# Optimization experiments

Hardware: AMD Instinct MI355X
Metric: run time of the kernel (lower is better)

Reference implementation:

```python
import jax, jax.numpy as jnp
import numpy as np

DIM = 1024
NUM_HEADS = 16


def setup_inputs() -> dict:
    key = jax.random.key(0)
    ks = jax.random.split(key, 6)
    B, N, C = 2, 2048, DIM
    x = jax.random.normal(ks[0], (B, N, C), dtype=jnp.float32)
    # torch nn.Linear weights have shape (out, in); qkv_bias=False, proj has bias
    wq = jax.random.normal(ks[1], (C, C), dtype=jnp.float32) * 0.02
    wk = jax.random.normal(ks[2], (C, C), dtype=jnp.float32) * 0.02
    wv = jax.random.normal(ks[3], (C, C), dtype=jnp.float32) * 0.02
    wp = jax.random.normal(ks[4], (C, C), dtype=jnp.float32) * 0.02
    bp = jax.random.normal(ks[5], (C,), dtype=jnp.float32) * 0.02
    return {"x": x, "wq": wq, "wk": wk, "wv": wv, "wp": wp, "bp": bp}


def reference(x, wq, wk, wv, wp, bp):
    B, N, C = x.shape
    H = NUM_HEADS
    D = C // H
    scale = D ** (-0.5)
    # projections (torch Linear: x @ W.T), split heads -> (B, H, N, D)
    q = (x @ wq.T).reshape(B, N, H, D).transpose(0, 2, 1, 3)
    k = (x @ wk.T).reshape(B, N, H, D).transpose(0, 2, 1, 3)
    v = (x @ wv.T).reshape(B, N, H, D).transpose(0, 2, 1, 3)
    # average keys over sequence -> (B, H, D)
    k_avg = k.mean(axis=2)
    # per-position logits against the single averaged key -> (B, H, N)
    z = jnp.einsum('bhnd,bhd->bhn', q, k_avg) * scale
    attn = jax.nn.softmax(z, axis=-1)  # (B, H, N); dropout is identity at eval
    # build circulant matrix: roll_weights[..., i, j] = attn[..., (j - i) mod N]
    pos = jnp.arange(N)
    idx = (pos[None, :] - pos[:, None]) % N  # (N, N)
    roll_weights = attn[:, :, idx]  # (B, H, N, N) gather-built circulant
    out = jnp.einsum('bhij,bhjd->bhid', roll_weights, v)  # (B, H, N, D)
    out = out.transpose(0, 2, 1, 3).reshape(B, N, C)
    return out @ wp.T + bp
```

## Files before the change

kernel.cpp:

```cpp
#include <hip/hip_runtime.h>
#include <stdint.h>

typedef unsigned short u16;
typedef __bf16 bf16x8 __attribute__((ext_vector_type(8)));
typedef float f32x4 __attribute__((ext_vector_type(4)));

static constexpr int kDim   = 1024;
static constexpr int kHeads = 16;
static constexpr int kN     = 2048;
static constexpr int kB     = 2;
static constexpr int kTok   = 4096;

static constexpr size_t OFF_XB   = 0;
static constexpr size_t OFF_VT   = OFF_XB   + (size_t)kTok*kDim*2;
static constexpr size_t OFF_OC   = OFF_VT   + (size_t)kTok*kDim*2;
static constexpr size_t OFF_WVB  = OFF_OC   + (size_t)kTok*kDim*2;
static constexpr size_t OFF_WPB  = OFF_WVB  + (size_t)kDim*kDim*2;
static constexpr size_t OFF_PART = OFF_WPB  + (size_t)kDim*kDim*2;
static constexpr size_t OFF_WZ   = OFF_PART + (size_t)kB*16*kDim*4;
static constexpr size_t OFF_Z    = OFF_WZ   + (size_t)kB*kHeads*kDim*4;
static constexpr size_t OFF_ATTN = OFF_Z    + (size_t)kB*kHeads*kN*4;
static constexpr int kAttnStride = 2064;

__device__ __forceinline__ u16 f2bf(float f) {
  unsigned int u = __builtin_bit_cast(unsigned int, f);
  u = (u + 0x7FFFu + ((u >> 16) & 1u)) >> 16;
  return (u16)u;
}

__device__ __forceinline__ void gload_lds16(const void* g, void* l) {
  __builtin_amdgcn_global_load_lds(
      (const __attribute__((address_space(1))) unsigned int*)g,
      (__attribute__((address_space(3))) unsigned int*)l, 16, 0, 0);
}

__global__ void cvtx_xsum_kernel(const float* __restrict__ x, u16* __restrict__ xb,
                                 float* __restrict__ part) {
  int bid = blockIdx.x;
  int cc = bid & 3, nc = (bid >> 2) & 15, b = bid >> 6;
  int tid = threadIdx.x, rg = tid >> 6, cl = tid & 63;
  int col = cc * 256 + cl * 4;
  size_t base = (size_t)b * kN + nc * 128;
  float4 s = make_float4(0.f, 0.f, 0.f, 0.f);
  for (int n = rg; n < 128; n += 4) {
    size_t idx = (base + n) * kDim + col;
    float4 v = *reinterpret_cast<const float4*>(&x[idx]);
    unsigned int lo = (unsigned int)f2bf(v.x) | ((unsigned int)f2bf(v.y) << 16);
    unsigned int hi = (unsigned int)f2bf(v.z) | ((unsigned int)f2bf(v.w) << 16);
    *reinterpret_cast<uint2*>(&xb[idx]) = make_uint2(lo, hi);
    s.x += v.x; s.y += v.y; s.z += v.z; s.w += v.w;
  }
  __shared__ float ps[4][256];
  ps[rg][cl * 4 + 0] = s.x; ps[rg][cl * 4 + 1] = s.y;
  ps[rg][cl * 4 + 2] = s.z; ps[rg][cl * 4 + 3] = s.w;
  __syncthreads();
  float tot = ps[0][tid] + ps[1][tid] + ps[2][tid] + ps[3][tid];
  part[((size_t)(b * 16 + nc)) * kDim + cc * 256 + tid] = tot;
}

__global__ void cvtw_kernel(const float* __restrict__ wv, const float* __restrict__ wp,
                            u16* __restrict__ out) {
  int i = blockIdx.x * 256 + threadIdx.x;
  const int half = kDim * kDim / 4;
  float4 f = (i < half) ? reinterpret_cast<const float4*>(wv)[i]
                        : reinterpret_cast<const float4*>(wp)[i - half];
  unsigned int lo = (unsigned int)f2bf(f.x) | ((unsigned int)f2bf(f.y) << 16);
  unsigned int hi = (unsigned int)f2bf(f.z) | ((unsigned int)f2bf(f.w) << 16);
  reinterpret_cast<uint2*>(out)[i] = make_uint2(lo, hi);
}

__global__ void kavgwz_kernel(const float* __restrict__ part, const float* __restrict__ wk,
                              const float* __restrict__ wq, float* __restrict__ wz) {
  int bh = blockIdx.x;
  int b = bh >> 4, h = bh & 15, tid = threadIdx.x;
  __shared__ float xsl[1024];
  __shared__ float kl[64];
  {
    f32x4 s = (f32x4){0.f, 0.f, 0.f, 0.f};
    for (int ch = 0; ch < 16; ++ch)
      s += *reinterpret_cast<const f32x4*>(&part[((size_t)(b * 16 + ch)) * kDim + tid * 4]);
    *reinterpret_cast<f32x4*>(&xsl[tid * 4]) = s;
  }
  __syncthreads();
  int d = tid >> 2, pt = tid & 3;
  const float* wkr = wk + (size_t)(h * 64 + d) * kDim;
  float s = 0.f;
  for (int k = pt; k < kDim; k += 4) s += xsl[k] * wkr[k];
  s += __shfl_xor(s, 1);
  s += __shfl_xor(s, 2);
  if (pt == 0) kl[d] = s * (1.0f / (float)kN);
  __syncthreads();
  float a0 = 0.f, a1 = 0.f, a2 = 0.f, a3 = 0.f;
  const float* wqb = wq + (size_t)h * 64 * kDim + tid;
  for (int dd = 0; dd < 64; ++dd) {
    float kd = kl[dd];
    const float* r = wqb + (size_t)dd * kDim;
    a0 += kd * r[0]; a1 += kd * r[256]; a2 += kd * r[512]; a3 += kd * r[768];
  }
  const float scale = 0.125f;
  float* o = wz + (size_t)bh * kDim + tid;
  o[0] = a0 * scale; o[256] = a1 * scale; o[512] = a2 * scale; o[768] = a3 * scale;
}

__global__ void z_kernel(const float* __restrict__ x, const float* __restrict__ wz,
                         float* __restrict__ z) {
  int blk = blockIdx.x;
  int b = blk >> 11, n = blk & 2047;
  __shared__ float xr[kDim];
  int tid = threadIdx.x, wid = tid >> 6, lane = tid & 63;
  reinterpret_cast<float4*>(xr)[tid] = reinterpret_cast<const float4*>(x + (size_t)blk * kDim)[tid];
  __syncthreads();
#pragma unroll
  for (int hh = 0; hh < 4; ++hh) {
    int h = wid * 4 + hh;
    const float* wzr = wz + (size_t)(b * kHeads + h) * kDim;
    float s = 0.f;
    for (int k = lane; k < kDim; k += 64) s += xr[k] * wzr[k];
#pragma unroll
    for (int off = 32; off; off >>= 1) s += __shfl_xor(s, off);
    if (lane == 0) z[(size_t)(b * kHeads + h) * kN + n] = s;
  }
}

__global__ void softmax_kernel(const float* __restrict__ z, u16* __restrict__ attn2) {
  int row = blockIdx.x, tid = threadIdx.x;
  int lane = tid & 63, wid = tid >> 6;
  const float* zr = z + (size_t)row * kN;
  float v[8];
  float mx = -1e30f;
#pragma unroll
  for (int j = 0; j < 8; ++j) { v[j] = zr[tid + j * 256]; mx = fmaxf(mx, v[j]); }
#pragma unroll
  for (int off = 32; off; off >>= 1) mx = fmaxf(mx, __shfl_xor(mx, off));
  __shared__ float redm[4], reds[4];
  if (lane == 0) redm[wid] = mx;
  __syncthreads();
  mx = fmaxf(fmaxf(redm[0], redm[1]), fmaxf(redm[2], redm[3]));
  float s = 0.f;
#pragma unroll
  for (int j = 0; j < 8; ++j) { v[j] = __expf(v[j] - mx); s += v[j]; }
#pragma unroll
  for (int off = 32; off; off >>= 1) s += __shfl_xor(s, off);
  if (lane == 0) reds[wid] = s;
  __syncthreads();
  s = reds[0] + reds[1] + reds[2] + reds[3];
  float inv = 1.0f / s;
  u16* out = attn2 + (size_t)row * kAttnStride;
#pragma unroll
  for (int j = 0; j < 8; ++j) out[tid + j * 256] = f2bf(v[j] * inv);
  if (tid < 8) out[2048 + tid] = f2bf(v[0] * inv);
}

template <int MODE>
__global__ __launch_bounds__(256, 2)
void gemm_bt_kernel(const u16* __restrict__ A, const u16* __restrict__ B,
                    void* __restrict__ Cout, const float* __restrict__ bias, int K) {
  __shared__ __align__(16) u16 As[2][128 * 64];
  __shared__ __align__(16) u16 Bs[2][64 * 64];
  int tid = threadIdx.x, lane = tid & 63, wid = tid >> 6;
  int wm = wid >> 1, wn = wid & 1;
  int lrow = lane & 15, kg = lane >> 4;
  int m0 = blockIdx.y * 128, n0 = blockIdx.x * 64;

  auto stage = [&](int buf, int k0) {
#pragma unroll
    for (int it = 0; it < 4; ++it) {
      int bchunk = it * 256 + wid * 64;
      int chunk = bchunk + lane;
      int row = chunk >> 3, cb = chunk & 7;
      int cs = cb ^ (row & 7);
      gload_lds16(A + (size_t)(m0 + row) * K + k0 + cs * 8, &As[buf][bchunk * 8]);
    }
#pragma unroll
    for (int it = 0; it < 2; ++it) {
      int bchunk = it * 256 + wid * 64;
      int chunk = bchunk + lane;
      int row = chunk >> 3, cb = chunk & 7;
      int cs = cb ^ (row & 7);
      gload_lds16(B + (size_t)(n0 + row) * K + k0 + cs * 8, &Bs[buf][bchunk * 8]);
    }
  };

  f32x4 acc[4][2];
#pragma unroll
  for (int i = 0; i < 4; ++i)
#pragma unroll
    for (int j = 0; j < 2; ++j) acc[i][j] = (f32x4){0.f, 0.f, 0.f, 0.f};

  stage(0, 0);
  __syncthreads();
  int buf = 0;
  for (int k0 = 0; k0 < K; k0 += 64) {
    if (k0 + 64 < K) stage(buf ^ 1, k0 + 64);
#pragma unroll
    for (int ks = 0; ks < 2; ++ks) {
      bf16x8 af[4], bfv[2];
#pragma unroll
      for (int mf = 0; mf < 4; ++mf) {
        int r = wm * 64 + mf * 16 + lrow;
        int c = (ks * 4 + kg) ^ (r & 7);
        af[mf] = *reinterpret_cast<const bf16x8*>(&As[buf][r * 64 + c * 8]);
      }
#pragma unroll
      for (int nf = 0; nf < 2; ++nf) {
        int r = wn * 32 + nf * 16 + lrow;
        int c = (ks * 4 + kg) ^ (r & 7);
        bfv[nf] = *reinterpret_cast<const bf16x8*>(&Bs[buf][r * 64 + c * 8]);
      }
#pragma unroll
      for (int mf = 0; mf < 4; ++mf)
#pragma unroll
        for (int nf = 0; nf < 2; ++nf)
          acc[mf][nf] = __builtin_amdgcn_mfma_f32_16x16x32_bf16(af[mf], bfv[nf], acc[mf][nf], 0, 0, 0);
    }
    __syncthreads();
    buf ^= 1;
  }

  if (MODE == 0) {
    u16* vT = (u16*)Cout;
#pragma unroll
    for (int mf = 0; mf < 4; ++mf) {
      int row0 = m0 + wm * 64 + mf * 16 + kg * 4;
      int bb = row0 >> 11, u = row0 & 2047;
#pragma unroll
      for (int nf = 0; nf < 2; ++nf) {
        int col = n0 + wn * 32 + nf * 16 + lrow;
        f32x4 a = acc[mf][nf];
        unsigned int lo = (unsigned int)f2bf(a.x) | ((unsigned int)f2bf(a.y) << 16);
        unsigned int hi = (unsigned int)f2bf(a.z) | ((unsigned int)f2bf(a.w) << 16);
        *reinterpret_cast<uint2*>(&vT[((size_t)(bb * kDim + col)) * kN + u]) = make_uint2(lo, hi);
      }
    }
  } else {
    float* y = (float*)Cout;
#pragma unroll
    for (int nf = 0; nf < 2; ++nf) {
      int col = n0 + wn * 32 + nf * 16 + lrow;
      float bv = bias[col];
#pragma unroll
      for (int mf = 0; mf < 4; ++mf) {
        int row0 = m0 + wm * 64 + mf * 16 + kg * 4;
        f32x4 a = acc[mf][nf];
        y[(size_t)(row0 + 0) * kDim + col] = a.x + bv;
        y[(size_t)(row0 + 1) * kDim + col] = a.y + bv;
        y[(size_t)(row0 + 2) * kDim + col] = a.z + bv;
        y[(size_t)(row0 + 3) * kDim + col] = a.w + bv;
      }
    }
  }
}

__global__ __launch_bounds__(256, 2)
void conv_kernel(const u16* __restrict__ vT, const u16* __restrict__ attn2,
                 u16* __restrict__ oc) {
  static constexpr int RS = 2056;
  __shared__ __align__(16) u16 reps[8 * RS];
  __shared__ __align__(16) u16 vts[2][64 * 64];
  int tid = threadIdx.x, lane = tid & 63, wid = tid >> 6;
  int wm = wid >> 1, wn = wid & 1;
  int lrow = lane & 15, kg = lane >> 4;
  int i0 = blockIdx.x * 128;
  int bh = blockIdx.y;
  int b = bh >> 4, h = bh & 15;

  const u16* arow = attn2 + (size_t)bh * kAttnStride;
  for (int p = 0; p < 8; ++p)
    for (int j = tid; j < 2048; j += 256) reps[p * RS + j] = arow[j + p];

  auto stage = [&](int buf, int u0) {
#pragma unroll
    for (int it = 0; it < 2; ++it) {
      int bchunk = it * 256 + wid * 64;
      int chunk = bchunk + lane;
      int d = chunk >> 3, cb = chunk & 7;
      int cs = cb ^ (d & 7);
      gload_lds16(vT + (size_t)(bh * 64 + d) * kN + u0 + cs * 8, &vts[buf][bchunk * 8]);
    }
  };

  f32x4 acc[2][4];
#pragma unroll
  for (int i = 0; i < 2; ++i)
#pragma unroll
    for (int j = 0; j < 4; ++j) acc[i][j] = (f32x4){0.f, 0.f, 0.f, 0.f};

  stage(0, 0);
  __syncthreads();
  int buf = 0;
  for (int u0 = 0; u0 < kN; u0 += 64) {
    if (u0 + 64 < kN) stage(buf ^ 1, u0 + 64);
#pragma unroll
    for (int ks = 0; ks < 2; ++ks) {
      bf16x8 af[2], bfv[4];
#pragma unroll
      for (int mf = 0; mf < 2; ++mf) {
        int r = wm * 32 + mf * 16 + lrow;
        int c = (ks * 4 + kg) ^ (r & 7);
        af[mf] = *reinterpret_cast<const bf16x8*>(&vts[buf][r * 64 + c * 8]);
      }
#pragma unroll
      for (int nf = 0; nf < 4; ++nf) {
        int i = i0 + wn * 64 + nf * 16 + lrow;
        int s = (u0 + ks * 32 + kg * 8 - i) & 2047;
        int p = s & 7;
        bfv[nf] = *reinterpret_cast<const bf16x8*>(&reps[p * RS + (s & ~7)]);
      }
#pragma unroll
      for (int mf = 0; mf < 2; ++mf)
#pragma unroll
        for (int nf = 0; nf < 4; ++nf)
          acc[mf][nf] = __builtin_amdgcn_mfma_f32_16x16x32_bf16(af[mf], bfv[nf], acc[mf][nf], 0, 0, 0);
    }
    __syncthreads();
    buf ^= 1;
  }

#pragma unroll
  for (int mf = 0; mf < 2; ++mf) {
    int d = wm * 32 + mf * 16 + kg * 4;
#pragma unroll
    for (int nf = 0; nf < 4; ++nf) {
      int i = i0 + wn * 64 + nf * 16 + lrow;
      f32x4 a = acc[mf][nf];
      unsigned int lo = (unsigned int)f2bf(a.x) | ((unsigned int)f2bf(a.y) << 16);
      unsigned int hi = (unsigned int)f2bf(a.z) | ((unsigned int)f2bf(a.w) << 16);
      *reinterpret_cast<uint2*>(&oc[((size_t)(b * kN + i)) * kDim + h * 64 + d]) = make_uint2(lo, hi);
    }
  }
}

extern "C" void kernel_launch(void* const* d_in, const int* in_sizes, int n_in,
                              void* d_out, int out_size, void* d_ws, size_t ws_size,
                              hipStream_t stream) {
  const float* x  = (const float*)d_in[0];
  const float* wq = (const float*)d_in[1];
  const float* wk = (const float*)d_in[2];
  const float* wv = (const float*)d_in[3];
  const float* wp = (const float*)d_in[4];
  const float* bp = (const float*)d_in[5];
  char* ws = (char*)d_ws;

  u16*   xb    = (u16*)(ws + OFF_XB);
  u16*   vTb   = (u16*)(ws + OFF_VT);
  u16*   ocb   = (u16*)(ws + OFF_OC);
  u16*   wvb   = (u16*)(ws + OFF_WVB);
  float* part  = (float*)(ws + OFF_PART);
  float* wz    = (float*)(ws + OFF_WZ);
  float* z     = (float*)(ws + OFF_Z);
  u16*   attn2 = (u16*)(ws + OFF_ATTN);
  u16*   wpb   = (u16*)(ws + OFF_WPB);

  cvtx_xsum_kernel<<<128, 256, 0, stream>>>(x, xb, part);
  cvtw_kernel<<<2048, 256, 0, stream>>>(wv, wp, wvb);
  kavgwz_kernel<<<32, 256, 0, stream>>>(part, wk, wq, wz);
  z_kernel<<<4096, 256, 0, stream>>>(x, wz, z);
  softmax_kernel<<<32, 256, 0, stream>>>(z, attn2);

  gemm_bt_kernel<0><<<dim3(16, 32), 256, 0, stream>>>(xb, wvb, vTb, nullptr, kDim);
  conv_kernel<<<dim3(16, 32), 256, 0, stream>>>(vTb, attn2, ocb);
  gemm_bt_kernel<1><<<dim3(16, 32), 256, 0, stream>>>(ocb, wpb, (float*)d_out, bp, kDim);
}
```

Before: 230.1 us.

## Split averaged-key and wz computation into three wider-parallel kernels

Replaces the single 32-block kavgwz kernel with three launches: a reduction of partial column sums, a 2048-block kernel computing each averaged-key element with one wavefront, and a 256-block kernel projecting the averaged key through wq. The old kernel ran only 32 blocks, each streaming a 64x1024 slice of wk and wq, which leaves most compute units idle. The split spreads that weight traffic across many more blocks, at the cost of two extra kernel launches and small intermediate buffers in the workspace.

```diff
diff --git a/kernel.cpp b/kernel.cpp
--- a/kernel.cpp
+++ b/kernel.cpp
@@ -17,7 +17,9 @@
 static constexpr size_t OFF_WVB  = OFF_OC   + (size_t)kTok*kDim*2;
 static constexpr size_t OFF_WPB  = OFF_WVB  + (size_t)kDim*kDim*2;
 static constexpr size_t OFF_PART = OFF_WPB  + (size_t)kDim*kDim*2;
-static constexpr size_t OFF_WZ   = OFF_PART + (size_t)kB*16*kDim*4;
+static constexpr size_t OFF_XS   = OFF_PART + (size_t)kB*16*kDim*4;
+static constexpr size_t OFF_KAVG = OFF_XS   + (size_t)kB*kDim*4;
+static constexpr size_t OFF_WZ   = OFF_KAVG + (size_t)kB*kHeads*64*4;
 static constexpr size_t OFF_Z    = OFF_WZ   + (size_t)kB*kHeads*kDim*4;
 static constexpr size_t OFF_ATTN = OFF_Z    + (size_t)kB*kHeads*kN*4;
 static constexpr int kAttnStride = 2064;
@@ -69,37 +71,41 @@
   reinterpret_cast<uint2*>(out)[i] = make_uint2(lo, hi);
 }
 
-__global__ void kavgwz_kernel(const float* __restrict__ part, const float* __restrict__ wk,
-                              const float* __restrict__ wq, float* __restrict__ wz) {
-  int bh = blockIdx.x;
-  int b = bh >> 4, h = bh & 15, tid = threadIdx.x;
-  __shared__ float xsl[1024];
+__global__ void xsumred_kernel(const float* __restrict__ part, float* __restrict__ xsum) {
+  int i = blockIdx.x * 256 + threadIdx.x;
+  int b = i >> 10, c = i & 1023;
+  float s = 0.f;
+#pragma unroll
+  for (int ch = 0; ch < 16; ++ch) s += part[((size_t)(b * 16 + ch)) * kDim + c];
+  xsum[i] = s;
+}
+
+__global__ void kavg_kernel(const float* __restrict__ xsum, const float* __restrict__ wk,
+                            float* __restrict__ kavg) {
+  int o = blockIdx.x;
+  int b = o >> 10;
+  int lane = threadIdx.x;
+  const float* wkr = wk + (size_t)(o & 1023) * kDim;
+  const float* xs = xsum + b * kDim;
+  float s = 0.f;
+  for (int k = lane; k < kDim; k += 64) s += xs[k] * wkr[k];
+#pragma unroll
+  for (int off = 32; off; off >>= 1) s += __shfl_xor(s, off);
+  if (lane == 0) kavg[o] = s * (1.0f / (float)kN);
+}
+
+__global__ void wz_kernel(const float* __restrict__ kavg, const float* __restrict__ wq,
+                          float* __restrict__ wz) {
+  int bh = blockIdx.x, h = bh & 15;
+  int col = blockIdx.y * 128 + threadIdx.x;
   __shared__ float kl[64];
-  {
-    f32x4 s = (f32x4){0.f, 0.f, 0.f, 0.f};
-    for (int ch = 0; ch < 16; ++ch)
-      s += *reinterpret_cast<const f32x4*>(&part[((size_t)(b * 16 + ch)) * kDim + tid * 4]);
-    *reinterpret_cast<f32x4*>(&xsl[tid * 4]) = s;
-  }
-  __syncthreads();
-  int d = tid >> 2, pt = tid & 3;
-  const float* wkr = wk + (size_t)(h * 64 + d) * kDim;
-  float s = 0.f;
-  for (int k = pt; k < kDim; k += 4) s += xsl[k] * wkr[k];
-  s += __shfl_xor(s, 1);
-  s += __shfl_xor(s, 2);
-  if (pt == 0) kl[d] = s * (1.0f / (float)kN);
-  __syncthreads();
-  float a0 = 0.f, a1 = 0.f, a2 = 0.f, a3 = 0.f;
-  const float* wqb = wq + (size_t)h * 64 * kDim + tid;
-  for (int dd = 0; dd < 64; ++dd) {
-    float kd = kl[dd];
-    const float* r = wqb + (size_t)dd * kDim;
-    a0 += kd * r[0]; a1 += kd * r[256]; a2 += kd * r[512]; a3 += kd * r[768];
-  }
-  const float scale = 0.125f;
-  float* o = wz + (size_t)bh * kDim + tid;
-  o[0] = a0 * scale; o[256] = a1 * scale; o[512] = a2 * scale; o[768] = a3 * scale;
+  if (threadIdx.x < 64) kl[threadIdx.x] = kavg[bh * 64 + threadIdx.x];
+  __syncthreads();
+  float a = 0.f;
+  const float* wqc = wq + (size_t)h * 64 * kDim + col;
+#pragma unroll
+  for (int dd = 0; dd < 64; ++dd) a += kl[dd] * wqc[(size_t)dd * kDim];
+  wz[(size_t)bh * kDim + col] = a * 0.125f;
 }
 
 __global__ void z_kernel(const float* __restrict__ x, const float* __restrict__ wz,
@@ -345,15 +351,19 @@
   u16*   vTb   = (u16*)(ws + OFF_VT);
   u16*   ocb   = (u16*)(ws + OFF_OC);
   u16*   wvb   = (u16*)(ws + OFF_WVB);
+  u16*   wpb   = (u16*)(ws + OFF_WPB);
   float* part  = (float*)(ws + OFF_PART);
+  float* xsum  = (float*)(ws + OFF_XS);
+  float* kavg  = (float*)(ws + OFF_KAVG);
   float* wz    = (float*)(ws + OFF_WZ);
   float* z     = (float*)(ws + OFF_Z);
   u16*   attn2 = (u16*)(ws + OFF_ATTN);
-  u16*   wpb   = (u16*)(ws + OFF_WPB);
 
   cvtx_xsum_kernel<<<128, 256, 0, stream>>>(x, xb, part);
   cvtw_kernel<<<2048, 256, 0, stream>>>(wv, wp, wvb);
-  kavgwz_kernel<<<32, 256, 0, stream>>>(part, wk, wq, wz);
+  xsumred_kernel<<<8, 256, 0, stream>>>(part, xsum);
+  kavg_kernel<<<2048, 64, 0, stream>>>(xsum, wk, kavg);
+  wz_kernel<<<dim3(32, 8), 128, 0, stream>>>(kavg, wq, wz);
   z_kernel<<<4096, 256, 0, stream>>>(x, wz, z);
   softmax_kernel<<<32, 256, 0, stream>>>(z, attn2);
 
```

After: 214.0 us. 7.0% less time.

## Fuse softmax into conv kernel, merge conversion kernels, split kwz columns

Applied to the files above, without the earlier changes.

Merges the x and weight bf16 conversion kernels into one launch, splits the k-average/wz kernel across four column chunks for more blocks, and folds the softmax into the conv kernel so each block computes the attention row from z and writes the shifted replicas straight into LDS. This drops two kernel launches and the attn2 global round trip. In exchange, each of the 512 conv blocks recomputes the full 2048-element softmax redundantly and does scattered LDS stores for the replicas.

```diff
diff --git a/kernel.cpp b/kernel.cpp
--- a/kernel.cpp
+++ b/kernel.cpp
@@ -19,8 +19,6 @@
 static constexpr size_t OFF_PART = OFF_WPB  + (size_t)kDim*kDim*2;
 static constexpr size_t OFF_WZ   = OFF_PART + (size_t)kB*16*kDim*4;
 static constexpr size_t OFF_Z    = OFF_WZ   + (size_t)kB*kHeads*kDim*4;
-static constexpr size_t OFF_ATTN = OFF_Z    + (size_t)kB*kHeads*kN*4;
-static constexpr int kAttnStride = 2064;
 
 __device__ __forceinline__ u16 f2bf(float f) {
   unsigned int u = __builtin_bit_cast(unsigned int, f);
@@ -34,10 +32,22 @@
       (__attribute__((address_space(3))) unsigned int*)l, 16, 0, 0);
 }
 
-__global__ void cvtx_xsum_kernel(const float* __restrict__ x, u16* __restrict__ xb,
-                                 float* __restrict__ part) {
+__global__ void cvt_all_kernel(const float* __restrict__ x, const float* __restrict__ wv,
+                               const float* __restrict__ wp, u16* __restrict__ xb,
+                               u16* __restrict__ wvb, float* __restrict__ part) {
   int bid = blockIdx.x;
-  int cc = bid & 3, nc = (bid >> 2) & 15, b = bid >> 6;
+  if (bid < 2048) {
+    int i = bid * 256 + threadIdx.x;
+    const int half = kDim * kDim / 4;
+    float4 f = (i < half) ? reinterpret_cast<const float4*>(wv)[i]
+                          : reinterpret_cast<const float4*>(wp)[i - half];
+    unsigned int lo = (unsigned int)f2bf(f.x) | ((unsigned int)f2bf(f.y) << 16);
+    unsigned int hi = (unsigned int)f2bf(f.z) | ((unsigned int)f2bf(f.w) << 16);
+    reinterpret_cast<uint2*>(wvb)[i] = make_uint2(lo, hi);
+    return;
+  }
+  int b2 = bid - 2048;
+  int cc = b2 & 3, nc = (b2 >> 2) & 15, b = b2 >> 6;
   int tid = threadIdx.x, rg = tid >> 6, cl = tid & 63;
   int col = cc * 256 + cl * 4;
   size_t base = (size_t)b * kN + nc * 128;
@@ -58,25 +68,16 @@
   part[((size_t)(b * 16 + nc)) * kDim + cc * 256 + tid] = tot;
 }
 
-__global__ void cvtw_kernel(const float* __restrict__ wv, const float* __restrict__ wp,
-                            u16* __restrict__ out) {
-  int i = blockIdx.x * 256 + threadIdx.x;
-  const int half = kDim * kDim / 4;
-  float4 f = (i < half) ? reinterpret_cast<const float4*>(wv)[i]
-                        : reinterpret_cast<const float4*>(wp)[i - half];
-  unsigned int lo = (unsigned int)f2bf(f.x) | ((unsigned int)f2bf(f.y) << 16);
-  unsigned int hi = (unsigned int)f2bf(f.z) | ((unsigned int)f2bf(f.w) << 16);
-  reinterpret_cast<uint2*>(out)[i] = make_uint2(lo, hi);
-}
-
-__global__ void kavgwz_kernel(const float* __restrict__ part, const float* __restrict__ wk,
-                              const float* __restrict__ wq, float* __restrict__ wz) {
-  int bh = blockIdx.x;
+__global__ void kwz_kernel(const float* __restrict__ part, const float* __restrict__ wk,
+                           const float* __restrict__ wq, float* __restrict__ wz) {
+  int blk = blockIdx.x;
+  int cc = blk & 3, bh = blk >> 2;
   int b = bh >> 4, h = bh & 15, tid = threadIdx.x;
   __shared__ float xsl[1024];
   __shared__ float kl[64];
   {
     f32x4 s = (f32x4){0.f, 0.f, 0.f, 0.f};
+#pragma unroll
     for (int ch = 0; ch < 16; ++ch)
       s += *reinterpret_cast<const f32x4*>(&part[((size_t)(b * 16 + ch)) * kDim + tid * 4]);
     *reinterpret_cast<f32x4*>(&xsl[tid * 4]) = s;
@@ -90,22 +91,18 @@
   s += __shfl_xor(s, 2);
   if (pt == 0) kl[d] = s * (1.0f / (float)kN);
   __syncthreads();
-  float a0 = 0.f, a1 = 0.f, a2 = 0.f, a3 = 0.f;
-  const float* wqb = wq + (size_t)h * 64 * kDim + tid;
-  for (int dd = 0; dd < 64; ++dd) {
-    float kd = kl[dd];
-    const float* r = wqb + (size_t)dd * kDim;
-    a0 += kd * r[0]; a1 += kd * r[256]; a2 += kd * r[512]; a3 += kd * r[768];
-  }
-  const float scale = 0.125f;
-  float* o = wz + (size_t)bh * kDim + tid;
-  o[0] = a0 * scale; o[256] = a1 * scale; o[512] = a2 * scale; o[768] = a3 * scale;
+  int col = cc * 256 + tid;
+  float a = 0.f;
+  const float* wqc = wq + (size_t)h * 64 * kDim + col;
+#pragma unroll
+  for (int dd = 0; dd < 64; ++dd) a += kl[dd] * wqc[(size_t)dd * kDim];
+  wz[(size_t)bh * kDim + col] = a * 0.125f;
 }
 
 __global__ void z_kernel(const float* __restrict__ x, const float* __restrict__ wz,
                          float* __restrict__ z) {
   int blk = blockIdx.x;
-  int b = blk >> 11, n = blk & 2047;
+  int b = blk >> 11;
   __shared__ float xr[kDim];
   int tid = threadIdx.x, wid = tid >> 6, lane = tid & 63;
   reinterpret_cast<float4*>(xr)[tid] = reinterpret_cast<const float4*>(x + (size_t)blk * kDim)[tid];
@@ -118,37 +115,8 @@
     for (int k = lane; k < kDim; k += 64) s += xr[k] * wzr[k];
 #pragma unroll
     for (int off = 32; off; off >>= 1) s += __shfl_xor(s, off);
-    if (lane == 0) z[(size_t)(b * kHeads + h) * kN + n] = s;
-  }
-}
-
-__global__ void softmax_kernel(const float* __restrict__ z, u16* __restrict__ attn2) {
-  int row = blockIdx.x, tid = threadIdx.x;
-  int lane = tid & 63, wid = tid >> 6;
-  const float* zr = z + (size_t)row * kN;
-  float v[8];
-  float mx = -1e30f;
-#pragma unroll
-  for (int j = 0; j < 8; ++j) { v[j] = zr[tid + j * 256]; mx = fmaxf(mx, v[j]); }
-#pragma unroll
-  for (int off = 32; off; off >>= 1) mx = fmaxf(mx, __shfl_xor(mx, off));
-  __shared__ float redm[4], reds[4];
-  if (lane == 0) redm[wid] = mx;
-  __syncthreads();
-  mx = fmaxf(fmaxf(redm[0], redm[1]), fmaxf(redm[2], redm[3]));
-  float s = 0.f;
-#pragma unroll
-  for (int j = 0; j < 8; ++j) { v[j] = __expf(v[j] - mx); s += v[j]; }
-#pragma unroll
-  for (int off = 32; off; off >>= 1) s += __shfl_xor(s, off);
-  if (lane == 0) reds[wid] = s;
-  __syncthreads();
-  s = reds[0] + reds[1] + reds[2] + reds[3];
-  float inv = 1.0f / s;
-  u16* out = attn2 + (size_t)row * kAttnStride;
-#pragma unroll
-  for (int j = 0; j < 8; ++j) out[tid + j * 256] = f2bf(v[j] * inv);
-  if (tid < 8) out[2048 + tid] = f2bf(v[0] * inv);
+    if (lane == 0) z[(size_t)(b * kHeads + h) * kN + (blk & 2047)] = s;
+  }
 }
 
 template <int MODE>
@@ -252,11 +220,12 @@
 }
 
 __global__ __launch_bounds__(256, 2)
-void conv_kernel(const u16* __restrict__ vT, const u16* __restrict__ attn2,
+void conv_kernel(const u16* __restrict__ vT, const float* __restrict__ z,
                  u16* __restrict__ oc) {
   static constexpr int RS = 2056;
   __shared__ __align__(16) u16 reps[8 * RS];
   __shared__ __align__(16) u16 vts[2][64 * 64];
+  __shared__ float redm[4], reds[4];
   int tid = threadIdx.x, lane = tid & 63, wid = tid >> 6;
   int wm = wid >> 1, wn = wid & 1;
   int lrow = lane & 15, kg = lane >> 4;
@@ -264,9 +233,34 @@
   int bh = blockIdx.y;
   int b = bh >> 4, h = bh & 15;
 
-  const u16* arow = attn2 + (size_t)bh * kAttnStride;
-  for (int p = 0; p < 8; ++p)
-    for (int j = tid; j < 2048; j += 256) reps[p * RS + j] = arow[j + p];
+  {
+    const float* zr = z + (size_t)bh * kN;
+    float vv[8];
+    float mx = -1e30f;
+#pragma unroll
+    for (int j = 0; j < 8; ++j) { vv[j] = zr[tid + j * 256]; mx = fmaxf(mx, vv[j]); }
+#pragma unroll
+    for (int off = 32; off; off >>= 1) mx = fmaxf(mx, __shfl_xor(mx, off));
+    if (lane == 0) redm[wid] = mx;
+    __syncthreads();
+    mx = fmaxf(fmaxf(redm[0], redm[1]), fmaxf(redm[2], redm[3]));
+    float s = 0.f;
+#pragma unroll
+    for (int j = 0; j < 8; ++j) { vv[j] = __expf(vv[j] - mx); s += vv[j]; }
+#pragma unroll
+    for (int off = 32; off; off >>= 1) s += __shfl_xor(s, off);
+    if (lane == 0) reds[wid] = s;
+    __syncthreads();
+    s = reds[0] + reds[1] + reds[2] + reds[3];
+    float inv = 1.0f / s;
+#pragma unroll
+    for (int j = 0; j < 8; ++j) {
+      u16 a = f2bf(vv[j] * inv);
+      int idx = tid + j * 256;
+#pragma unroll
+      for (int p = 0; p < 8; ++p) reps[p * RS + ((idx - p) & 2047)] = a;
+    }
+  }
 
   auto stage = [&](int buf, int u0) {
 #pragma unroll
@@ -345,19 +339,15 @@
   u16*   vTb   = (u16*)(ws + OFF_VT);
   u16*   ocb   = (u16*)(ws + OFF_OC);
   u16*   wvb   = (u16*)(ws + OFF_WVB);
+  u16*   wpb   = (u16*)(ws + OFF_WPB);
   float* part  = (float*)(ws + OFF_PART);
   float* wz    = (float*)(ws + OFF_WZ);
   float* z     = (float*)(ws + OFF_Z);
-  u16*   attn2 = (u16*)(ws + OFF_ATTN);
-  u16*   wpb   = (u16*)(ws + OFF_WPB);
-
-  cvtx_xsum_kernel<<<128, 256, 0, stream>>>(x, xb, part);
-  cvtw_kernel<<<2048, 256, 0, stream>>>(wv, wp, wvb);
-  kavgwz_kernel<<<32, 256, 0, stream>>>(part, wk, wq, wz);
+
+  cvt_all_kernel<<<2176, 256, 0, stream>>>(x, wv, wp, xb, wvb, part);
+  kwz_kernel<<<128, 256, 0, stream>>>(part, wk, wq, wz);
   z_kernel<<<4096, 256, 0, stream>>>(x, wz, z);
-  softmax_kernel<<<32, 256, 0, stream>>>(z, attn2);
-
   gemm_bt_kernel<0><<<dim3(16, 32), 256, 0, stream>>>(xb, wvb, vTb, nullptr, kDim);
-  conv_kernel<<<dim3(16, 32), 256, 0, stream>>>(vTb, attn2, ocb);
+  conv_kernel<<<dim3(16, 32), 256, 0, stream>>>(vTb, z, ocb);
   gemm_bt_kernel<1><<<dim3(16, 32), 256, 0, stream>>>(ocb, wpb, (float*)d_out, bp, kDim);
 }
```

New measurement: 231.0 us. No clear change (+0.4%).
